# Kernel tuning notes

Measured on AMD Instinct MI355X. Metric: run time of the kernel, lower is better.

Reference implementation:

```python
import jax, jax.numpy as jnp
import numpy as np

BSZ, SEQ, T, ENC, HID = 32, 2048, 32, 512, 512


def setup_inputs() -> dict:
    key = jax.random.key(0)
    ks = jax.random.split(key, 8)
    L = SEQ // T  # uniform turn length -> end ids cover every token
    end_ids = jnp.broadcast_to((jnp.arange(T, dtype=jnp.int32) + 1) * L - 1, (BSZ, T))
    s = 1.0 / np.sqrt(HID)
    return {
        "encoder_output": jax.random.normal(ks[0], (BSZ, SEQ, ENC), jnp.float32),
        "end_ids": end_ids,
        "W_ih": jax.random.uniform(ks[1], (4 * HID, ENC), jnp.float32, -s, s),
        "W_hh": jax.random.uniform(ks[2], (4 * HID, HID), jnp.float32, -s, s),
        "b_ih": jax.random.uniform(ks[3], (4 * HID,), jnp.float32, -s, s),
        "b_hh": jax.random.uniform(ks[4], (4 * HID,), jnp.float32, -s, s),
        "fc_w": jax.random.uniform(ks[5], (1, HID + ENC), jnp.float32, -s, s),
        "fc_b": jnp.zeros((1,), jnp.float32),
    }


def reference(encoder_output, end_ids, W_ih, W_hh, b_ih, b_hh, fc_w, fc_b):
    bsz, S, E = encoder_output.shape
    Tn = end_ids.shape[1]
    H = W_hh.shape[1]

    # ---- ragged segment-mean pooling: token t in turn j iff prev_end < t <= end[j]
    tok = jnp.arange(S)
    seg = jax.vmap(lambda e: jnp.searchsorted(e, tok))(end_ids)  # [bsz,S]
    gid = (seg + jnp.arange(bsz)[:, None] * Tn).reshape(-1)
    sums = jax.ops.segment_sum(encoder_output.reshape(-1, E), gid, num_segments=bsz * Tn)
    starts = jnp.concatenate([jnp.zeros((bsz, 1), end_ids.dtype), end_ids[:, :-1] + 1], axis=1)
    counts = (end_ids - starts + 1).astype(encoder_output.dtype)  # [bsz,Tn]
    turn_states = sums.reshape(bsz, Tn, E) / counts[..., None]

    # ---- all sliding windows of 3 consecutive turns
    J = Tn - 3
    widx = jnp.arange(J)[:, None] + jnp.arange(3)[None, :]  # [J,3]
    src = turn_states[:, widx].reshape(bsz * J, 3, E)  # [N,3,E]

    # ---- single-layer LSTM (pytorch gate order i,f,g,o), take last hidden state
    bias = b_ih + b_hh

    def step(carry, x_t):
        h, c = carry
        g = x_t @ W_ih.T + h @ W_hh.T + bias
        i_, f_, g_, o_ = jnp.split(g, 4, axis=-1)
        c = jax.nn.sigmoid(f_) * c + jax.nn.sigmoid(i_) * jnp.tanh(g_)
        h = jax.nn.sigmoid(o_) * jnp.tanh(c)
        return (h, c), None

    h0 = jnp.zeros((bsz * J, H), src.dtype)
    (hT, _), _ = jax.lax.scan(step, (h0, h0), jnp.swapaxes(src, 0, 1))

    # ---- con_fc([src_last, tgt]) decomposes into src-part + tgt-part of the weight
    sscore = (hT @ fc_w[0, :H]).reshape(bsz, J)  # [bsz,J]
    tscore = turn_states @ fc_w[0, H:]  # [bsz,Tn]
    kidx = jnp.arange(J)[:, None] + 3 + jnp.arange(J)[None, :]  # [J,J] candidate turn ids
    valid = kidx < Tn
    kc = jnp.clip(kidx, 0, Tn - 1)
    logits = sscore[:, :, None] + tscore[:, kc] + fc_b[0]  # [bsz,J,J]
    logits = jnp.where(valid[None], logits, jnp.float32(-1e9))
    # cross entropy with target index 0 (the j+3 turn is the positive)
    loss = jax.nn.logsumexp(logits, axis=-1) - logits[..., 0]  # [bsz,J]
    return jnp.mean(loss)
```

## Files before the change

kernel.cpp:

```cpp
#include <hip/hip_runtime.h>
#include <math.h>

#define BSZ   32
#define SEQL  2048
#define TN    32
#define ENCD  512
#define HIDD  512
#define JW    29
#define NW    (BSZ * JW)

typedef short bf16x8 __attribute__((ext_vector_type(8)));
typedef float f32x4  __attribute__((ext_vector_type(4)));

__device__ __forceinline__ float sigm(float x) { return 1.f / (1.f + expf(-x)); }

__device__ __forceinline__ unsigned short f2bf(float x) {
    union { float f; unsigned u; } v; v.f = x;
    unsigned u = v.u;
    u += 0x7FFF + ((u >> 16) & 1);
    return (unsigned short)(u >> 16);
}
__device__ __forceinline__ float bf2f(short s) {
    union { unsigned u; float f; } v; v.u = ((unsigned)(unsigned short)s) << 16;
    return v.f;
}

#define GLOAD_LDS16(gp, lp)                                                    \
    __builtin_amdgcn_global_load_lds(                                          \
        (const __attribute__((address_space(1))) void*)(gp),                   \
        (__attribute__((address_space(3))) void*)(lp), 16, 0, 0)

__global__ __launch_bounds__(512) void prep_k(const float* __restrict__ enc,
                                              const int* __restrict__ end_ids,
                                              short* __restrict__ tsbf,
                                              const float* __restrict__ w1,
                                              const float* __restrict__ w2,
                                              short* __restrict__ o1,
                                              short* __restrict__ o2,
                                              const float* __restrict__ fcw,
                                              float* __restrict__ tsc) {
    int tid = threadIdx.x;
    int bid = blockIdx.x;
    if (bid >= 1024) {
        int idx = (bid - 1024) * 512 + tid;
        int t = idx >> 17;
        int i = idx & 131071;
        const float* s = (t ? w2 : w1) + (size_t)i * 8;
        short* o = (t ? o2 : o1) + (size_t)i * 8;
        float4 a = ((const float4*)s)[0];
        float4 b = ((const float4*)s)[1];
        union { short v[8]; bf16x8 p; } r;
        r.v[0] = (short)f2bf(a.x); r.v[1] = (short)f2bf(a.y);
        r.v[2] = (short)f2bf(a.z); r.v[3] = (short)f2bf(a.w);
        r.v[4] = (short)f2bf(b.x); r.v[5] = (short)f2bf(b.y);
        r.v[6] = (short)f2bf(b.z); r.v[7] = (short)f2bf(b.w);
        *(bf16x8*)o = r.p;
        return;
    }
    int j = bid & 31;
    int b = bid >> 5;
    int e_end   = end_ids[bid];
    int e_start = j ? (end_ids[bid - 1] + 1) : 0;
    int col = (tid & 127) << 2;
    int tr  = tid >> 7;
    const float* base = enc + (size_t)b * SEQL * ENCD + col;
    float ax = 0.f, ay = 0.f, az = 0.f, aw = 0.f;
    float bx = 0.f, by = 0.f, bz = 0.f, bw = 0.f;
    for (int t = e_start + tr; t <= e_end; t += 8) {
        float4 v = *(const float4*)(base + (size_t)t * ENCD);
        ax += v.x; ay += v.y; az += v.z; aw += v.w;
        int t2 = t + 4;
        if (t2 <= e_end) {
            float4 u = *(const float4*)(base + (size_t)t2 * ENCD);
            bx += u.x; by += u.y; bz += u.z; bw += u.w;
        }
    }
    ax += bx; ay += by; az += bz; aw += bw;
    __shared__ float4 part[3][128];
    __shared__ float red[128];
    if (tr) part[tr - 1][tid & 127] = make_float4(ax, ay, az, aw);
    __syncthreads();
    if (!tr) {
        float4 p0 = part[0][tid], p1 = part[1][tid], p2 = part[2][tid];
        float inv = 1.f / (float)(e_end - e_start + 1);
        float mx = (ax + p0.x + p1.x + p2.x) * inv;
        float my = (ay + p0.y + p1.y + p2.y) * inv;
        float mz = (az + p0.z + p1.z + p2.z) * inv;
        float mw = (aw + p0.w + p1.w + p2.w) * inv;
        union { unsigned short v[4]; uint2 p; } q;
        q.v[0] = f2bf(mx); q.v[1] = f2bf(my); q.v[2] = f2bf(mz); q.v[3] = f2bf(mw);
        *(uint2*)(tsbf + (size_t)bid * ENCD + col) = q.p;
        float4 wv = *(const float4*)(fcw + HIDD + col);
        red[tid] = mx * wv.x + my * wv.y + mz * wv.z + mw * wv.w;
    }
    __syncthreads();
    if (tid < 64) {
        float s = red[tid] + red[tid + 64];
#pragma unroll
        for (int sh = 32; sh; sh >>= 1) s += __shfl_down(s, sh, 64);
        if (tid == 0) tsc[bid] = s;
    }
}

template <int STEP>
__global__ __launch_bounds__(256) void gemm_lstm(const short* __restrict__ A,
                                                 const short* __restrict__ B,
                                                 ushort4* __restrict__ XWq,
                                                 float* __restrict__ Cb,
                                                 short* __restrict__ Hout,
                                                 float* __restrict__ ss_part,
                                                 const float* __restrict__ b_ih,
                                                 const float* __restrict__ b_hh,
                                                 const float* __restrict__ fcw) {
    __shared__ short Als[2][4 * 512];
    __shared__ short Bls[2][16 * 512];
    int tid = threadIdx.x, w = tid >> 6, lane = tid & 63;
    int l15 = lane & 15, l4 = lane >> 4;
    int m0 = blockIdx.y * 32, hcol0 = blockIdx.x * 32;
    int wm = (w >> 1) * 16, wh = (w & 1) * 16;
    int hcol = hcol0 + wh + l15;
    const short* Aptr = A + (size_t)m0 * 512;
    f32x4 acc[4] = {};

    auto stage = [&](int sel, int k0) {
#pragma unroll
        for (int i = 0; i < 5; ++i) {
            int c = w * 5 + i;
            if (c < 4) {
                int unit = c * 64 + lane;
                int row = unit >> 3, slot = unit & 7;
                int scol = slot ^ (row & 7);
                GLOAD_LDS16(Aptr + (size_t)row * 512 + k0 + scol * 8,
                            &Als[sel][c * 512]);
            } else {
                int cc = c - 4;
                int unit = cc * 64 + lane;
                int rr = unit >> 3, slot = unit & 7;
                int grow = (rr >> 5) * 512 + hcol0 + (rr & 31);
                int scol = slot ^ (rr & 7);
                GLOAD_LDS16(B + (size_t)grow * 512 + k0 + scol * 8,
                            &Bls[sel][cc * 512]);
            }
        }
    };

    stage(0, 0);
    __syncthreads();
    int sel = 0;
    for (int t = 0; t < 8; ++t) {
        if (t < 7) stage(sel ^ 1, (t + 1) * 64);
        bf16x8 af[2], bfr[4][2];
#pragma unroll
        for (int kk = 0; kk < 2; ++kk) {
            int row = wm + l15;
            int s = (kk * 4 + l4) ^ (row & 7);
            af[kk] = *(const bf16x8*)&Als[sel][row * 64 + s * 8];
#pragma unroll
            for (int g = 0; g < 4; ++g) {
                int rr = g * 32 + wh + l15;
                int s2 = (kk * 4 + l4) ^ (rr & 7);
                bfr[g][kk] = *(const bf16x8*)&Bls[sel][rr * 64 + s2 * 8];
            }
        }
#pragma unroll
        for (int kk = 0; kk < 2; ++kk)
#pragma unroll
            for (int g = 0; g < 4; ++g)
                acc[g] = __builtin_amdgcn_mfma_f32_16x16x32_bf16(
                    af[kk], bfr[g][kk], acc[g], 0, 0, 0);
        __syncthreads();
        sel ^= 1;
    }

    float bb0, bb1, bb2, bb3;
    if (STEP == 1) {
        bb0 = b_ih[hcol]        + b_hh[hcol];
        bb1 = b_ih[512 + hcol]  + b_hh[512 + hcol];
        bb2 = b_ih[1024 + hcol] + b_hh[1024 + hcol];
        bb3 = b_ih[1536 + hcol] + b_hh[1536 + hcol];
    }
    float hreg[4];
#pragma unroll
    for (int r = 0; r < 4; ++r) {
        int row = m0 + wm + l4 * 4 + r;
        float gi = acc[0][r], gf = acc[1][r];
        float gg = acc[2][r], go = acc[3][r];
        float cn;
        if (STEP == 1) {
            gi += bb0; gf += bb1; gg += bb2; go += bb3;
            ushort4 q;
            q.x = f2bf(gi); q.y = f2bf(gf); q.z = f2bf(gg); q.w = f2bf(go);
            XWq[(size_t)row * 512 + hcol] = q;
            cn = sigm(gi) * tanhf(gg);
        } else {
            int xr = row + (STEP - 1); if (xr > 1023) xr = 1023;
            ushort4 q = XWq[(size_t)xr * 512 + hcol];
            gi += bf2f((short)q.x); gf += bf2f((short)q.y);
            gg += bf2f((short)q.z); go += bf2f((short)q.w);
            cn = sigm(gf) * Cb[(size_t)row * 512 + hcol] + sigm(gi) * tanhf(gg);
        }
        float h = sigm(go) * tanhf(cn);
        if (STEP < 3) {
            Cb[(size_t)row * 512 + hcol] = cn;
            Hout[(size_t)row * 512 + hcol] = (short)f2bf(h);
        } else {
            hreg[r] = h;
        }
    }
    if (STEP == 3) {
        float fcv = fcw[hcol];
        float* sred = (float*)&Als[0][0];
        float vals[4];
#pragma unroll
        for (int r = 0; r < 4; ++r) {
            float v = hreg[r] * fcv;
#pragma unroll
            for (int m = 1; m < 16; m <<= 1) v += __shfl_xor(v, m, 64);
            vals[r] = v;
        }
        __syncthreads();
        if ((w & 1) == 0 && l15 == 0)
#pragma unroll
            for (int r = 0; r < 4; ++r) sred[wm + l4 * 4 + r] = vals[r];
        __syncthreads();
        if ((w & 1) == 1 && l15 == 0)
#pragma unroll
            for (int r = 0; r < 4; ++r) sred[wm + l4 * 4 + r] += vals[r];
        __syncthreads();
        if (tid < 32) ss_part[(size_t)(m0 + tid) * 16 + blockIdx.x] = sred[tid];
    }
}

__global__ __launch_bounds__(1024) void loss_k(const float* __restrict__ ss_part,
                                               const float* __restrict__ tsc,
                                               const float* __restrict__ fcb,
                                               float* __restrict__ out) {
    int tid = threadIdx.x;
    float l = 0.f;
    if (tid < NW) {
        int b = tid / JW, j = tid - (tid / JW) * JW;
        int turn = b * TN + j;
        const float* sp = ss_part + (size_t)turn * 16;
        float s = 0.f;
#pragma unroll
        for (int k = 0; k < 16; ++k) s += sp[k];
        float base = s + fcb[0];
        int nv = JW - j;
        const float* tp = tsc + b * TN + j + 3;
        float m = -1e30f, l0 = 0.f;
        for (int k = 0; k < nv; ++k) {
            float lg = base + tp[k];
            if (k == 0) l0 = lg;
            m = fmaxf(m, lg);
        }
        float sum = 0.f;
        for (int k = 0; k < nv; ++k) sum += expf(base + tp[k] - m);
        l = (m + logf(sum)) - l0;
    }
    __shared__ float red[16];
#pragma unroll
    for (int s = 32; s; s >>= 1) l += __shfl_down(l, s, 64);
    int wid = tid >> 6, lane = tid & 63;
    if (lane == 0) red[wid] = l;
    __syncthreads();
    if (tid == 0) {
        float tot = 0.f;
        for (int i = 0; i < 16; ++i) tot += red[i];
        out[0] = tot / (float)NW;
    }
}

extern "C" void kernel_launch(void* const* d_in, const int* in_sizes, int n_in,
                              void* d_out, int out_size, void* d_ws, size_t ws_size,
                              hipStream_t stream) {
    const float* enc     = (const float*)d_in[0];
    const int*   end_ids = (const int*)d_in[1];
    const float* W_ih    = (const float*)d_in[2];
    const float* W_hh    = (const float*)d_in[3];
    const float* b_ih    = (const float*)d_in[4];
    const float* b_hh    = (const float*)d_in[5];
    const float* fc_w    = (const float*)d_in[6];
    const float* fc_b    = (const float*)d_in[7];
    float* out = (float*)d_out;

    short* tsbf   = (short*)d_ws;
    short* Wih_bf = tsbf + 1024 * 512;
    short* Whh_bf = Wih_bf + 2048 * 512;
    short* HA     = Whh_bf + 2048 * 512;
    short* HB     = HA + 1024 * 512;
    ushort4* XWq  = (ushort4*)(HB + 1024 * 512);
    float* Cb     = (float*)(XWq + 1024 * 512);
    float* ss_part = Cb + 1024 * 512;
    float* tsc    = ss_part + 1024 * 16;

    prep_k<<<1536, 512, 0, stream>>>(enc, end_ids, tsbf, W_ih, W_hh,
                                     Wih_bf, Whh_bf, fc_w, tsc);
    gemm_lstm<1><<<dim3(16, 32), 256, 0, stream>>>(tsbf, Wih_bf, XWq, Cb, HA,
                                                   nullptr, b_ih, b_hh, fc_w);
    gemm_lstm<2><<<dim3(16, 32), 256, 0, stream>>>(HA, Whh_bf, XWq, Cb, HB,
                                                   nullptr, b_ih, b_hh, fc_w);
    gemm_lstm<3><<<dim3(16, 32), 256, 0, stream>>>(HB, Whh_bf, XWq, Cb, nullptr,
                                                   ss_part, b_ih, b_hh, fc_w);
    loss_k<<<1, 1024, 0, stream>>>(ss_part, tsc, fc_b, out);
}
```

Baseline: 66.56 us.

## Fuse loss into last LSTM step via last-block atomic and tighten GEMM barriers

Result: slower. 98.59 us (+48.1%).

```diff
diff --git a/kernel.cpp b/kernel.cpp
--- a/kernel.cpp
+++ b/kernel.cpp
@@ -38,10 +38,12 @@
                                               short* __restrict__ o1,
                                               short* __restrict__ o2,
                                               const float* __restrict__ fcw,
-                                              float* __restrict__ tsc) {
+                                              float* __restrict__ tsc,
+                                              unsigned* __restrict__ done) {
     int tid = threadIdx.x;
     int bid = blockIdx.x;
     if (bid >= 1024) {
+        if (bid == 1024 && tid == 0) done[0] = 0;
         int idx = (bid - 1024) * 512 + tid;
         int t = idx >> 17;
         int i = idx & 131071;
@@ -111,7 +113,11 @@
                                                  float* __restrict__ ss_part,
                                                  const float* __restrict__ b_ih,
                                                  const float* __restrict__ b_hh,
-                                                 const float* __restrict__ fcw) {
+                                                 const float* __restrict__ fcw,
+                                                 const float* __restrict__ tsc,
+                                                 const float* __restrict__ fcb,
+                                                 unsigned* __restrict__ done,
+                                                 float* __restrict__ out) {
     __shared__ short Als[2][4 * 512];
     __shared__ short Bls[2][16 * 512];
     int tid = threadIdx.x, w = tid >> 6, lane = tid & 63;
@@ -145,10 +151,17 @@
     };
 
     stage(0, 0);
-    __syncthreads();
     int sel = 0;
+#pragma unroll
     for (int t = 0; t < 8; ++t) {
-        if (t < 7) stage(sel ^ 1, (t + 1) * 64);
+        if (t < 7) {
+            stage(sel ^ 1, (t + 1) * 64);
+            asm volatile("s_waitcnt vmcnt(5)" ::: "memory");
+        } else {
+            asm volatile("s_waitcnt vmcnt(0)" ::: "memory");
+        }
+        __builtin_amdgcn_s_barrier();
+        __builtin_amdgcn_sched_barrier(0);
         bf16x8 af[2], bfr[4][2];
 #pragma unroll
         for (int kk = 0; kk < 2; ++kk) {
@@ -162,13 +175,15 @@
                 bfr[g][kk] = *(const bf16x8*)&Bls[sel][rr * 64 + s2 * 8];
             }
         }
+        asm volatile("s_waitcnt lgkmcnt(0)" ::: "memory");
+        __builtin_amdgcn_sched_barrier(0);
+        __builtin_amdgcn_s_barrier();
 #pragma unroll
         for (int kk = 0; kk < 2; ++kk)
 #pragma unroll
             for (int g = 0; g < 4; ++g)
                 acc[g] = __builtin_amdgcn_mfma_f32_16x16x32_bf16(
                     af[kk], bfr[g][kk], acc[g], 0, 0, 0);
-        __syncthreads();
         sel ^= 1;
     }
 
@@ -228,45 +243,46 @@
             for (int r = 0; r < 4; ++r) sred[wm + l4 * 4 + r] += vals[r];
         __syncthreads();
         if (tid < 32) ss_part[(size_t)(m0 + tid) * 16 + blockIdx.x] = sred[tid];
-    }
-}
-
-__global__ __launch_bounds__(1024) void loss_k(const float* __restrict__ ss_part,
-                                               const float* __restrict__ tsc,
-                                               const float* __restrict__ fcb,
-                                               float* __restrict__ out) {
-    int tid = threadIdx.x;
-    float l = 0.f;
-    if (tid < NW) {
-        int b = tid / JW, j = tid - (tid / JW) * JW;
-        int turn = b * TN + j;
-        const float* sp = ss_part + (size_t)turn * 16;
-        float s = 0.f;
-#pragma unroll
-        for (int k = 0; k < 16; ++k) s += sp[k];
-        float base = s + fcb[0];
-        int nv = JW - j;
-        const float* tp = tsc + b * TN + j + 3;
-        float m = -1e30f, l0 = 0.f;
-        for (int k = 0; k < nv; ++k) {
-            float lg = base + tp[k];
-            if (k == 0) l0 = lg;
-            m = fmaxf(m, lg);
-        }
-        float sum = 0.f;
-        for (int k = 0; k < nv; ++k) sum += expf(base + tp[k] - m);
-        l = (m + logf(sum)) - l0;
-    }
-    __shared__ float red[16];
-#pragma unroll
-    for (int s = 32; s; s >>= 1) l += __shfl_down(l, s, 64);
-    int wid = tid >> 6, lane = tid & 63;
-    if (lane == 0) red[wid] = l;
-    __syncthreads();
-    if (tid == 0) {
-        float tot = 0.f;
-        for (int i = 0; i < 16; ++i) tot += red[i];
-        out[0] = tot / (float)NW;
+
+        __shared__ unsigned win;
+        __syncthreads();
+        if (tid == 0) {
+            __threadfence();
+            unsigned old = atomicAdd(done, 1u);
+            win = (old == 511u) ? 1u : 0u;
+            __threadfence();
+        }
+        __syncthreads();
+        if (win) {
+            float l = 0.f;
+            for (int n = tid; n < NW; n += 256) {
+                int b = n / JW, j = n - (n / JW) * JW;
+                int turn = b * TN + j;
+                const float* sp = ss_part + (size_t)turn * 16;
+                float s = 0.f;
+#pragma unroll
+                for (int k = 0; k < 16; ++k) s += sp[k];
+                float base = s + fcb[0];
+                int nv = JW - j;
+                const float* tp = tsc + b * TN + j + 3;
+                float m = -1e30f, l0 = 0.f;
+                for (int k = 0; k < nv; ++k) {
+                    float lg = base + tp[k];
+                    if (k == 0) l0 = lg;
+                    m = fmaxf(m, lg);
+                }
+                float sum = 0.f;
+                for (int k = 0; k < nv; ++k) sum += expf(base + tp[k] - m);
+                l += (m + logf(sum)) - l0;
+            }
+#pragma unroll
+            for (int sh = 32; sh; sh >>= 1) l += __shfl_down(l, sh, 64);
+            float* red2 = (float*)&Bls[0][0];
+            if (lane == 0) red2[w] = l;
+            __syncthreads();
+            if (tid == 0)
+                out[0] = (red2[0] + red2[1] + red2[2] + red2[3]) / (float)NW;
+        }
     }
 }
 
@@ -292,14 +308,17 @@
     float* Cb     = (float*)(XWq + 1024 * 512);
     float* ss_part = Cb + 1024 * 512;
     float* tsc    = ss_part + 1024 * 16;
+    unsigned* done = (unsigned*)(tsc + 1024);
 
     prep_k<<<1536, 512, 0, stream>>>(enc, end_ids, tsbf, W_ih, W_hh,
-                                     Wih_bf, Whh_bf, fc_w, tsc);
+                                     Wih_bf, Whh_bf, fc_w, tsc, done);
     gemm_lstm<1><<<dim3(16, 32), 256, 0, stream>>>(tsbf, Wih_bf, XWq, Cb, HA,
-                                                   nullptr, b_ih, b_hh, fc_w);
+                                                   nullptr, b_ih, b_hh, fc_w,
+                                                   tsc, fc_b, done, out);
     gemm_lstm<2><<<dim3(16, 32), 256, 0, stream>>>(HA, Whh_bf, XWq, Cb, HB,
-                                                   nullptr, b_ih, b_hh, fc_w);
+                                                   nullptr, b_ih, b_hh, fc_w,
+                                                   tsc, fc_b, done, out);
     gemm_lstm<3><<<dim3(16, 32), 256, 0, stream>>>(HB, Whh_bf, XWq, Cb, nullptr,
-                                                   ss_part, b_ih, b_hh, fc_w);
-    loss_k<<<1, 1024, 0, stream>>>(ss_part, tsc, fc_b, out);
-}
+                                                   ss_part, b_ih, b_hh, fc_w,
+                                                   tsc, fc_b, done, out);
+}
```

## Fuse three LSTM step kernels into one with per-row-block semaphores

Applied to the files above, without the earlier changes.

Measured after the change: 202.9 us. 205% more time.

```diff
diff --git a/kernel.cpp b/kernel.cpp
--- a/kernel.cpp
+++ b/kernel.cpp
@@ -38,10 +38,12 @@
                                               short* __restrict__ o1,
                                               short* __restrict__ o2,
                                               const float* __restrict__ fcw,
-                                              float* __restrict__ tsc) {
+                                              float* __restrict__ tsc,
+                                              unsigned* __restrict__ sem) {
     int tid = threadIdx.x;
     int bid = blockIdx.x;
     if (bid >= 1024) {
+        if (bid == 1024) { sem[tid] = 0; sem[tid + 512] = 0; }
         int idx = (bid - 1024) * 512 + tid;
         int t = idx >> 17;
         int i = idx & 131071;
@@ -102,133 +104,159 @@
     }
 }
 
-template <int STEP>
-__global__ __launch_bounds__(256) void gemm_lstm(const short* __restrict__ A,
-                                                 const short* __restrict__ B,
-                                                 ushort4* __restrict__ XWq,
-                                                 float* __restrict__ Cb,
-                                                 short* __restrict__ Hout,
-                                                 float* __restrict__ ss_part,
-                                                 const float* __restrict__ b_ih,
-                                                 const float* __restrict__ b_hh,
-                                                 const float* __restrict__ fcw) {
+__device__ __forceinline__ void waitsem(unsigned* s, unsigned target) {
+    while (__hip_atomic_load(s, __ATOMIC_RELAXED, __HIP_MEMORY_SCOPE_AGENT)
+           < target)
+        __builtin_amdgcn_s_sleep(2);
+}
+
+__global__ __launch_bounds__(256) void gemm_all(const short* __restrict__ tsbf,
+                                                const short* __restrict__ Wih,
+                                                const short* __restrict__ Whh,
+                                                ushort4* __restrict__ XWq,
+                                                short* __restrict__ HA,
+                                                short* __restrict__ HB,
+                                                float* __restrict__ ss_part,
+                                                const float* __restrict__ b_ih,
+                                                const float* __restrict__ b_hh,
+                                                const float* __restrict__ fcw,
+                                                unsigned* __restrict__ sem) {
     __shared__ short Als[2][4 * 512];
     __shared__ short Bls[2][16 * 512];
     int tid = threadIdx.x, w = tid >> 6, lane = tid & 63;
     int l15 = lane & 15, l4 = lane >> 4;
     int m0 = blockIdx.y * 32, hcol0 = blockIdx.x * 32;
+    int by = blockIdx.y;
     int wm = (w >> 1) * 16, wh = (w & 1) * 16;
     int hcol = hcol0 + wh + l15;
-    const short* Aptr = A + (size_t)m0 * 512;
-    f32x4 acc[4] = {};
-
-    auto stage = [&](int sel, int k0) {
-#pragma unroll
-        for (int i = 0; i < 5; ++i) {
-            int c = w * 5 + i;
-            if (c < 4) {
-                int unit = c * 64 + lane;
-                int row = unit >> 3, slot = unit & 7;
-                int scol = slot ^ (row & 7);
-                GLOAD_LDS16(Aptr + (size_t)row * 512 + k0 + scol * 8,
-                            &Als[sel][c * 512]);
+    float bb0 = b_ih[hcol]        + b_hh[hcol];
+    float bb1 = b_ih[512 + hcol]  + b_hh[512 + hcol];
+    float bb2 = b_ih[1024 + hcol] + b_hh[1024 + hcol];
+    float bb3 = b_ih[1536 + hcol] + b_hh[1536 + hcol];
+    float creg[4];
+    float hreg[4];
+
+    for (int step = 1; step <= 3; ++step) {
+        const short* A = (step == 1) ? tsbf : (step == 2 ? HA : HB);
+        const short* B = (step == 1) ? Wih : Whh;
+        const short* Aptr = A + (size_t)m0 * 512;
+        f32x4 acc[4] = {};
+
+        auto stage = [&](int sel, int k0) {
+#pragma unroll
+            for (int i = 0; i < 5; ++i) {
+                int c = w * 5 + i;
+                if (c < 4) {
+                    int unit = c * 64 + lane;
+                    int row = unit >> 3, slot = unit & 7;
+                    int scol = slot ^ (row & 7);
+                    GLOAD_LDS16(Aptr + (size_t)row * 512 + k0 + scol * 8,
+                                &Als[sel][c * 512]);
+                } else {
+                    int cc = c - 4;
+                    int unit = cc * 64 + lane;
+                    int rr = unit >> 3, slot = unit & 7;
+                    int grow = (rr >> 5) * 512 + hcol0 + (rr & 31);
+                    int scol = slot ^ (rr & 7);
+                    GLOAD_LDS16(B + (size_t)grow * 512 + k0 + scol * 8,
+                                &Bls[sel][cc * 512]);
+                }
+            }
+        };
+
+        stage(0, 0);
+        __syncthreads();
+        int sel = 0;
+        for (int t = 0; t < 8; ++t) {
+            if (t < 7) stage(sel ^ 1, (t + 1) * 64);
+            bf16x8 af[2], bfr[4][2];
+#pragma unroll
+            for (int kk = 0; kk < 2; ++kk) {
+                int row = wm + l15;
+                int s = (kk * 4 + l4) ^ (row & 7);
+                af[kk] = *(const bf16x8*)&Als[sel][row * 64 + s * 8];
+#pragma unroll
+                for (int g = 0; g < 4; ++g) {
+                    int rr = g * 32 + wh + l15;
+                    int s2 = (kk * 4 + l4) ^ (rr & 7);
+                    bfr[g][kk] = *(const bf16x8*)&Bls[sel][rr * 64 + s2 * 8];
+                }
+            }
+#pragma unroll
+            for (int kk = 0; kk < 2; ++kk)
+#pragma unroll
+                for (int g = 0; g < 4; ++g)
+                    acc[g] = __builtin_amdgcn_mfma_f32_16x16x32_bf16(
+                        af[kk], bfr[g][kk], acc[g], 0, 0, 0);
+            __syncthreads();
+            sel ^= 1;
+        }
+
+#pragma unroll
+        for (int r = 0; r < 4; ++r) {
+            int row = m0 + wm + l4 * 4 + r;
+            float gi = acc[0][r], gf = acc[1][r];
+            float gg = acc[2][r], go = acc[3][r];
+            float cn;
+            if (step == 1) {
+                gi += bb0; gf += bb1; gg += bb2; go += bb3;
+                ushort4 q;
+                q.x = f2bf(gi); q.y = f2bf(gf); q.z = f2bf(gg); q.w = f2bf(go);
+                XWq[(size_t)row * 512 + hcol] = q;
+                cn = sigm(gi) * tanhf(gg);
             } else {
-                int cc = c - 4;
-                int unit = cc * 64 + lane;
-                int rr = unit >> 3, slot = unit & 7;
-                int grow = (rr >> 5) * 512 + hcol0 + (rr & 31);
-                int scol = slot ^ (rr & 7);
-                GLOAD_LDS16(B + (size_t)grow * 512 + k0 + scol * 8,
-                            &Bls[sel][cc * 512]);
+                int xr = row + (step - 1); if (xr > 1023) xr = 1023;
+                ushort4 q = XWq[(size_t)xr * 512 + hcol];
+                gi += bf2f((short)q.x); gf += bf2f((short)q.y);
+                gg += bf2f((short)q.z); go += bf2f((short)q.w);
+                cn = sigm(gf) * creg[r] + sigm(gi) * tanhf(gg);
             }
-        }
-    };
-
-    stage(0, 0);
-    __syncthreads();
-    int sel = 0;
-    for (int t = 0; t < 8; ++t) {
-        if (t < 7) stage(sel ^ 1, (t + 1) * 64);
-        bf16x8 af[2], bfr[4][2];
-#pragma unroll
-        for (int kk = 0; kk < 2; ++kk) {
-            int row = wm + l15;
-            int s = (kk * 4 + l4) ^ (row & 7);
-            af[kk] = *(const bf16x8*)&Als[sel][row * 64 + s * 8];
-#pragma unroll
-            for (int g = 0; g < 4; ++g) {
-                int rr = g * 32 + wh + l15;
-                int s2 = (kk * 4 + l4) ^ (rr & 7);
-                bfr[g][kk] = *(const bf16x8*)&Bls[sel][rr * 64 + s2 * 8];
+            creg[r] = cn;
+            float h = sigm(go) * tanhf(cn);
+            if (step == 1)      HA[(size_t)row * 512 + hcol] = (short)f2bf(h);
+            else if (step == 2) HB[(size_t)row * 512 + hcol] = (short)f2bf(h);
+            else                hreg[r] = h;
+        }
+
+        if (step < 3) {
+            asm volatile("s_waitcnt vmcnt(0)" ::: "memory");
+            __threadfence();
+            __syncthreads();
+            if (tid == 0) {
+                unsigned* s0 = sem + (step - 1) * 512 + by * 16;
+                __hip_atomic_fetch_add(s0, 1u, __ATOMIC_RELAXED,
+                                       __HIP_MEMORY_SCOPE_AGENT);
+                waitsem(s0, 16);
+                if (step == 1) {
+                    int byp = (by < 31) ? by + 1 : 31;
+                    waitsem(sem + byp * 16, 16);
+                }
             }
-        }
-#pragma unroll
-        for (int kk = 0; kk < 2; ++kk)
-#pragma unroll
-            for (int g = 0; g < 4; ++g)
-                acc[g] = __builtin_amdgcn_mfma_f32_16x16x32_bf16(
-                    af[kk], bfr[g][kk], acc[g], 0, 0, 0);
-        __syncthreads();
-        sel ^= 1;
-    }
-
-    float bb0, bb1, bb2, bb3;
-    if (STEP == 1) {
-        bb0 = b_ih[hcol]        + b_hh[hcol];
-        bb1 = b_ih[512 + hcol]  + b_hh[512 + hcol];
-        bb2 = b_ih[1024 + hcol] + b_hh[1024 + hcol];
-        bb3 = b_ih[1536 + hcol] + b_hh[1536 + hcol];
-    }
-    float hreg[4];
+            __syncthreads();
+            __threadfence();
+        }
+    }
+
+    float fcv = fcw[hcol];
+    float* sred = (float*)&Als[0][0];
+    float vals[4];
 #pragma unroll
     for (int r = 0; r < 4; ++r) {
-        int row = m0 + wm + l4 * 4 + r;
-        float gi = acc[0][r], gf = acc[1][r];
-        float gg = acc[2][r], go = acc[3][r];
-        float cn;
-        if (STEP == 1) {
-            gi += bb0; gf += bb1; gg += bb2; go += bb3;
-            ushort4 q;
-            q.x = f2bf(gi); q.y = f2bf(gf); q.z = f2bf(gg); q.w = f2bf(go);
-            XWq[(size_t)row * 512 + hcol] = q;
-            cn = sigm(gi) * tanhf(gg);
-        } else {
-            int xr = row + (STEP - 1); if (xr > 1023) xr = 1023;
-            ushort4 q = XWq[(size_t)xr * 512 + hcol];
-            gi += bf2f((short)q.x); gf += bf2f((short)q.y);
-            gg += bf2f((short)q.z); go += bf2f((short)q.w);
-            cn = sigm(gf) * Cb[(size_t)row * 512 + hcol] + sigm(gi) * tanhf(gg);
-        }
-        float h = sigm(go) * tanhf(cn);
-        if (STEP < 3) {
-            Cb[(size_t)row * 512 + hcol] = cn;
-            Hout[(size_t)row * 512 + hcol] = (short)f2bf(h);
-        } else {
-            hreg[r] = h;
-        }
-    }
-    if (STEP == 3) {
-        float fcv = fcw[hcol];
-        float* sred = (float*)&Als[0][0];
-        float vals[4];
-#pragma unroll
-        for (int r = 0; r < 4; ++r) {
-            float v = hreg[r] * fcv;
-#pragma unroll
-            for (int m = 1; m < 16; m <<= 1) v += __shfl_xor(v, m, 64);
-            vals[r] = v;
-        }
-        __syncthreads();
-        if ((w & 1) == 0 && l15 == 0)
-#pragma unroll
-            for (int r = 0; r < 4; ++r) sred[wm + l4 * 4 + r] = vals[r];
-        __syncthreads();
-        if ((w & 1) == 1 && l15 == 0)
-#pragma unroll
-            for (int r = 0; r < 4; ++r) sred[wm + l4 * 4 + r] += vals[r];
-        __syncthreads();
-        if (tid < 32) ss_part[(size_t)(m0 + tid) * 16 + blockIdx.x] = sred[tid];
-    }
+        float v = hreg[r] * fcv;
+#pragma unroll
+        for (int m = 1; m < 16; m <<= 1) v += __shfl_xor(v, m, 64);
+        vals[r] = v;
+    }
+    __syncthreads();
+    if ((w & 1) == 0 && l15 == 0)
+#pragma unroll
+        for (int r = 0; r < 4; ++r) sred[wm + l4 * 4 + r] = vals[r];
+    __syncthreads();
+    if ((w & 1) == 1 && l15 == 0)
+#pragma unroll
+        for (int r = 0; r < 4; ++r) sred[wm + l4 * 4 + r] += vals[r];
+    __syncthreads();
+    if (tid < 32) ss_part[(size_t)(m0 + tid) * 16 + blockIdx.x] = sred[tid];
 }
 
 __global__ __launch_bounds__(1024) void loss_k(const float* __restrict__ ss_part,
@@ -289,17 +317,14 @@
     short* HA     = Whh_bf + 2048 * 512;
     short* HB     = HA + 1024 * 512;
     ushort4* XWq  = (ushort4*)(HB + 1024 * 512);
-    float* Cb     = (float*)(XWq + 1024 * 512);
-    float* ss_part = Cb + 1024 * 512;
+    float* ss_part = (float*)(XWq + 1024 * 512);
     float* tsc    = ss_part + 1024 * 16;
+    unsigned* sem = (unsigned*)(tsc + 1024);
 
     prep_k<<<1536, 512, 0, stream>>>(enc, end_ids, tsbf, W_ih, W_hh,
-                                     Wih_bf, Whh_bf, fc_w, tsc);
-    gemm_lstm<1><<<dim3(16, 32), 256, 0, stream>>>(tsbf, Wih_bf, XWq, Cb, HA,
-                                                   nullptr, b_ih, b_hh, fc_w);
-    gemm_lstm<2><<<dim3(16, 32), 256, 0, stream>>>(HA, Whh_bf, XWq, Cb, HB,
-                                                   nullptr, b_ih, b_hh, fc_w);
-    gemm_lstm<3><<<dim3(16, 32), 256, 0, stream>>>(HB, Whh_bf, XWq, Cb, nullptr,
-                                                   ss_part, b_ih, b_hh, fc_w);
+                                     Wih_bf, Whh_bf, fc_w, tsc, sem);
+    gemm_all<<<dim3(16, 32), 256, 0, stream>>>(tsbf, Wih_bf, Whh_bf, XWq,
+                                               HA, HB, ss_part, b_ih, b_hh,
+                                               fc_w, sem);
     loss_k<<<1, 1024, 0, stream>>>(ss_part, tsc, fc_b, out);
 }
```
